# Kernel optimization log

Hardware: AMD Instinct MI355X
Metric: run time of the kernel (lower is better)

Reference implementation:

```python
import jax, jax.numpy as jnp
import numpy as np

N_NODES = 50000
N_EDGES = 1600000
D_IN = 192   # n_features + n_graphfea
D_HID = 128


def _gcn_conv(x, W, b, src, dst, dhis, n):
    """GCNConv returning two views.
    view1: symmetric-normalized propagation with self-loops (standard GCN).
    view2: raw neighbor sum of transformed features (to be scaled by D_inv outside).
    dhis: deg_hat^{-1/2} per node, deg_hat = in-degree + 1 (self loop).
    """
    h = x @ W + b                                      # [N, hid]
    w = dhis[src] * dhis[dst]                          # [E] edge norm
    view1 = jax.ops.segment_sum(h[src] * w[:, None], dst, num_segments=n)
    view1 = view1 + h * (dhis * dhis)[:, None]         # self-loop term
    view2 = jax.ops.segment_sum(h[src], dst, num_segments=n)
    return view1, view2


def setup_inputs() -> dict:
    key = jax.random.key(0)
    ks = jax.random.split(key, 12)
    x = jax.random.normal(ks[0], (N_NODES, D_IN), dtype=jnp.float32)
    view2 = jax.random.normal(ks[1], (N_NODES, D_IN), dtype=jnp.float32)
    edge_index = jax.random.randint(ks[2], (2, N_EDGES), 0, N_NODES, dtype=jnp.int64)
    D_inv = jax.random.uniform(ks[3], (N_NODES, 1), dtype=jnp.float32)
    def glorot(k, fan_in, fan_out):
        s = jnp.sqrt(jnp.float32(2.0 / (fan_in + fan_out)))
        return jax.random.normal(k, (fan_in, fan_out), dtype=jnp.float32) * s
    W1 = glorot(ks[4], D_IN, D_HID)
    W2 = glorot(ks[5], D_HID, D_HID)
    W3 = glorot(ks[6], D_HID, D_HID)
    W4 = glorot(ks[7], D_IN, D_HID)
    W5 = glorot(ks[8], D_HID, D_HID)
    W6 = glorot(ks[9], D_HID, D_HID)
    z = jnp.zeros((D_HID,), dtype=jnp.float32)
    return {"x": x, "view2": view2, "edge_index": edge_index, "D_inv": D_inv,
            "W1": W1, "b1": z, "W2": W2, "b2": z, "W3": W3, "b3": z,
            "W4": W4, "b4": z, "W5": W5, "b5": z, "W6": W6, "b6": z}


def reference(x, view2, edge_index, D_inv,
              W1, b1, W2, b2, W3, b3, W4, b4, W5, b5, W6, b6):
    n = x.shape[0]
    src, dst = edge_index[0], edge_index[1]
    deg = jax.ops.segment_sum(jnp.ones_like(dst, dtype=x.dtype), dst, num_segments=n)
    dhis = jax.lax.rsqrt(deg + 1.0)                    # deg_hat^{-1/2}
    relu = jax.nn.relu

    x1v1, x1v2 = _gcn_conv(x, W1, b1, src, dst, dhis, n)
    x2v1, x2v2 = _gcn_conv(view2, W4, b4, src, dst, dhis, n)
    x1 = relu(x1v1 + x2v2 * D_inv)
    x2 = relu(x2v1 + x1v2 * D_inv)

    z1v1, z1v2 = _gcn_conv(x1, W2, b2, src, dst, dhis, n)
    z2v1, z2v2 = _gcn_conv(x2, W5, b5, src, dst, dhis, n)
    z1 = relu(z1v1 + z2v2 * D_inv)
    z2 = relu(z2v1 + z1v2 * D_inv)

    v1v1, v1v2 = _gcn_conv(z1, W3, b3, src, dst, dhis, n)
    v2v1, v2v2 = _gcn_conv(z2, W6, b6, src, dst, dhis, n)
    v1 = relu(v1v1 + v2v2 * D_inv)
    v2 = relu(v2v1 + v1v2 * D_inv)

    q = jnp.concatenate([x1, z1, v1], axis=1)          # [N, 3*hid]
    p = jnp.concatenate([x2, z2, v2], axis=1)
    return q, p
```

## Files before the change

### kernel.cpp

```cpp
#include <hip/hip_runtime.h>

#define N_NODES 50000
#define N_EDGES 1600000
#define D_IN 192
#define D_HID 128

#define NSLICE 8
#define SLICE_SZ ((N_NODES + NSLICE - 1) / NSLICE)

typedef __bf16 bf16x8 __attribute__((ext_vector_type(8)));
typedef float f32x4 __attribute__((ext_vector_type(4)));
typedef float f32x2 __attribute__((ext_vector_type(2)));
typedef unsigned short u16x8 __attribute__((ext_vector_type(8)));

__device__ __forceinline__ unsigned short f2b(float x) {
    unsigned u = __builtin_bit_cast(unsigned, x);
    u += 0x7FFFu + ((u >> 16) & 1u);
    return (unsigned short)(u >> 16);
}
__device__ __forceinline__ float blo(unsigned u) {
    return __builtin_bit_cast(float, u << 16);
}
__device__ __forceinline__ float bhi(unsigned u) {
    return __builtin_bit_cast(float, u & 0xFFFF0000u);
}
__device__ __forceinline__ bf16x8 pack8(float4 a, float4 b) {
    u16x8 t;
    t[0] = f2b(a.x); t[1] = f2b(a.y); t[2] = f2b(a.z); t[3] = f2b(a.w);
    t[4] = f2b(b.x); t[5] = f2b(b.y); t[6] = f2b(b.z); t[7] = f2b(b.w);
    return __builtin_bit_cast(bf16x8, t);
}


__global__ void hist_kernel(const int* __restrict__ dst, int E,
                            int* __restrict__ cnt, int* __restrict__ rank) {
    int e = blockIdx.x * blockDim.x + threadIdx.x;
    if (e < E) rank[e] = atomicAdd(&cnt[dst[e]], 1);
}

__global__ __launch_bounds__(256) void scanA(const int* __restrict__ cnt,
                                             int* __restrict__ bsum, int n) {
    int i = blockIdx.x * 256 + threadIdx.x;
    int v = (i < n) ? cnt[i] : 0;
#pragma unroll
    for (int off = 32; off > 0; off >>= 1) v += __shfl_down(v, off);
    __shared__ int ws[4];
    if ((threadIdx.x & 63) == 0) ws[threadIdx.x >> 6] = v;
    __syncthreads();
    if (threadIdx.x == 0) bsum[blockIdx.x] = ws[0] + ws[1] + ws[2] + ws[3];
}

__global__ __launch_bounds__(256) void scanB(const int* __restrict__ bsum,
                                             int* __restrict__ boff,
                                             int* __restrict__ row_ptr, int nb, int n) {
    __shared__ int s[256];
    int tid = threadIdx.x;
    int v = (tid < nb) ? bsum[tid] : 0;
    s[tid] = v;
    __syncthreads();
    for (int off = 1; off < 256; off <<= 1) {
        int add = (tid >= off) ? s[tid - off] : 0;
        __syncthreads();
        s[tid] += add;
        __syncthreads();
    }
    if (tid < nb) boff[tid] = (tid > 0) ? s[tid - 1] : 0;
    if (tid == 0) row_ptr[n] = s[255];
}

__global__ __launch_bounds__(256) void scanC(const int* __restrict__ cnt,
                                             const int* __restrict__ boff,
                                             int* __restrict__ row_ptr,
                                             float* __restrict__ dhis, int n) {
    __shared__ int s[256];
    int tid = threadIdx.x;
    int i = blockIdx.x * 256 + tid;
    int c = (i < n) ? cnt[i] : 0;
    s[tid] = c;
    __syncthreads();
    for (int off = 1; off < 256; off <<= 1) {
        int add = (tid >= off) ? s[tid - off] : 0;
        __syncthreads();
        s[tid] += add;
        __syncthreads();
    }
    if (i < n) {
        int pre = boff[blockIdx.x] + s[tid] - c;
        row_ptr[i] = pre;
        dhis[i] = rsqrtf((float)c + 1.0f);
    }
}

__global__ __launch_bounds__(256) void fill_sliced(
        const int* __restrict__ src, const int* __restrict__ dst,
        const int* __restrict__ rank, const int* __restrict__ row_ptr,
        int* __restrict__ esrc, int E, int nchunks) {
    int slice = blockIdx.x & (NSLICE - 1);
    int chunk = blockIdx.x >> 3;
    int lo = slice * SLICE_SZ;
    int hi = lo + SLICE_SZ;
    int per = (E + nchunks - 1) / nchunks;
    int e0 = chunk * per;
    int e1 = min(e0 + per, E);
    for (int e = e0 + threadIdx.x; e < e1; e += 256) {
        int d = dst[e];
        if (d >= lo && d < hi) {
            esrc[row_ptr[d] + rank[e]] = src[e];
        }
    }
}


__global__ void prep_all(const float* __restrict__ W1, const float* __restrict__ W4,
                         const float* __restrict__ W2, const float* __restrict__ W3,
                         const float* __restrict__ W5, const float* __restrict__ W6,
                         unsigned short* __restrict__ Wt) {
    int idx = blockIdx.x * 256 + threadIdx.x;
    const float* W; int K, base;
    if      (idx <  24576) { W = W1; K = 192; base = 0; }
    else if (idx <  49152) { W = W4; K = 192; base = 24576; }
    else if (idx <  65536) { W = W2; K = 128; base = 49152; }
    else if (idx <  81920) { W = W3; K = 128; base = 65536; }
    else if (idx <  98304) { W = W5; K = 128; base = 81920; }
    else if (idx < 114688) { W = W6; K = 128; base = 98304; }
    else return;
    int r = idx - base;
    int j = r / K, k = r - j * K;
    Wt[idx] = f2b(W[(size_t)k * 128 + j]);
}


__global__ __launch_bounds__(256) void gemm_dual(
        const float* __restrict__ A0, const float* __restrict__ A1, int lda,
        int K, int ns,
        const unsigned short* __restrict__ Wt0, const unsigned short* __restrict__ Wt1,
        const float* __restrict__ bias0, const float* __restrict__ bias1,
        unsigned short* __restrict__ out, int M) {
    __shared__ __align__(16) unsigned short Wlds[192 * 128];

    int view = blockIdx.y;
    const float* A = view ? A1 : A0;
    const unsigned short* Wt = view ? Wt1 : Wt0;
    const float* bias = view ? bias1 : bias0;

    int tid = threadIdx.x;

    int nfrag = ns * 512;
    for (int f = tid; f < nfrag; f += 256) {
        int lane = f & 63;
        int gk = f >> 6;
        int g = gk / ns, ks = gk - g * ns;
        int col = g * 16 + (lane & 15);
        int kpos = ks * 32 + (lane >> 4) * 8;
        *(bf16x8*)(Wlds + (size_t)f * 8) =
            *(const bf16x8*)(Wt + (size_t)col * K + kpos);
    }
    __syncthreads();

    int wave = tid >> 6, lane = tid & 63;
    int m = lane & 15, quad = lane >> 4;
    int row0 = blockIdx.x * 128;

    int rA0 = row0 + wave * 32 + m;
    int rA1 = rA0 + 16;
    int cA0 = rA0 < M ? rA0 : M - 1;
    int cA1 = rA1 < M ? rA1 : M - 1;
    const float* a0 = A + (size_t)cA0 * lda + quad * 8;
    const float* a1 = A + (size_t)cA1 * lda + quad * 8;

    f32x4 acc[2][8];
#pragma unroll
    for (int h = 0; h < 2; ++h)
#pragma unroll
        for (int g = 0; g < 8; ++g) acc[h][g] = (f32x4){0.f, 0.f, 0.f, 0.f};

    const bf16x8* wl = (const bf16x8*)Wlds;
    for (int ks = 0; ks < ns; ++ks) {
        float4 va = *(const float4*)(a0 + ks * 32);
        float4 vb = *(const float4*)(a0 + ks * 32 + 4);
        float4 vc = *(const float4*)(a1 + ks * 32);
        float4 vd = *(const float4*)(a1 + ks * 32 + 4);
        bf16x8 af0 = pack8(va, vb);
        bf16x8 af1 = pack8(vc, vd);
#pragma unroll
        for (int g = 0; g < 8; ++g) {
            bf16x8 bfr = wl[(g * ns + ks) * 64 + lane];
            acc[0][g] = __builtin_amdgcn_mfma_f32_16x16x32_bf16(af0, bfr, acc[0][g], 0, 0, 0);
            acc[1][g] = __builtin_amdgcn_mfma_f32_16x16x32_bf16(af1, bfr, acc[1][g], 0, 0, 0);
        }
    }

#pragma unroll
    for (int h = 0; h < 2; ++h) {
#pragma unroll
        for (int g = 0; g < 8; ++g) {
            int col = g * 16 + m;
            float bv = bias[col];
            int ci = ((col >> 1) << 2) + (view << 1) + (col & 1);
#pragma unroll
            for (int r = 0; r < 4; ++r) {
                int grow = row0 + wave * 32 + h * 16 + quad * 4 + r;
                if (grow < M) out[(size_t)grow * 256 + ci] = f2b(acc[h][g][r] + bv);
            }
        }
    }
}


__global__ __launch_bounds__(256) void agg_kernel(
        const unsigned* __restrict__ hcomb,
        const int* __restrict__ row_ptr, const int* __restrict__ esrc,
        const float* __restrict__ dhis, const float* __restrict__ D_inv,
        float* __restrict__ out_q, float* __restrict__ out_p, int n) {
    int wave = threadIdx.x >> 6, lane = threadIdx.x & 63;
    int d = blockIdx.x * 4 + wave;
    if (d >= n) return;

    const uint2* hc2 = (const uint2*)hcomb;

    int e0 = row_ptr[d], e1 = row_ptr[d + 1];
    f32x2 a1 = {0.f, 0.f}, g1 = {0.f, 0.f};
    f32x2 a2 = {0.f, 0.f}, g2 = {0.f, 0.f};

#define EDGE_BODY(u, w) {                                         \
        f32x2 v1 = {blo((u).x), bhi((u).x)};                      \
        f32x2 v2 = {blo((u).y), bhi((u).y)};                      \
        f32x2 wv = {(w), (w)};                                    \
        a1 += v1; g1 = __builtin_elementwise_fma(v1, wv, g1);     \
        a2 += v2; g2 = __builtin_elementwise_fma(v2, wv, g2); }

    int e = e0;
    for (; e + 8 <= e1; e += 8) {
        int4 sa = *(const int4*)(esrc + e);
        int4 sb = *(const int4*)(esrc + e + 4);
        uint2 u0 = hc2[((size_t)sa.x << 6) + lane];
        uint2 u1 = hc2[((size_t)sa.y << 6) + lane];
        uint2 u2 = hc2[((size_t)sa.z << 6) + lane];
        uint2 u3 = hc2[((size_t)sa.w << 6) + lane];
        uint2 u4 = hc2[((size_t)sb.x << 6) + lane];
        uint2 u5 = hc2[((size_t)sb.y << 6) + lane];
        uint2 u6 = hc2[((size_t)sb.z << 6) + lane];
        uint2 u7 = hc2[((size_t)sb.w << 6) + lane];
        float w0 = dhis[sa.x], w1 = dhis[sa.y], w2 = dhis[sa.z], w3 = dhis[sa.w];
        float w4 = dhis[sb.x], w5 = dhis[sb.y], w6 = dhis[sb.z], w7 = dhis[sb.w];
        EDGE_BODY(u0, w0); EDGE_BODY(u1, w1);
        EDGE_BODY(u2, w2); EDGE_BODY(u3, w3);
        EDGE_BODY(u4, w4); EDGE_BODY(u5, w5);
        EDGE_BODY(u6, w6); EDGE_BODY(u7, w7);
    }
    for (; e + 4 <= e1; e += 4) {
        int4 sa = *(const int4*)(esrc + e);
        uint2 u0 = hc2[((size_t)sa.x << 6) + lane];
        uint2 u1 = hc2[((size_t)sa.y << 6) + lane];
        uint2 u2 = hc2[((size_t)sa.z << 6) + lane];
        uint2 u3 = hc2[((size_t)sa.w << 6) + lane];
        float w0 = dhis[sa.x], w1 = dhis[sa.y], w2 = dhis[sa.z], w3 = dhis[sa.w];
        EDGE_BODY(u0, w0); EDGE_BODY(u1, w1);
        EDGE_BODY(u2, w2); EDGE_BODY(u3, w3);
    }
    for (; e < e1; ++e) {
        int s = esrc[e];
        uint2 u = hc2[((size_t)s << 6) + lane];
        EDGE_BODY(u, dhis[s]);
    }
#undef EDGE_BODY

    float dh = dhis[d];
    float di = D_inv[d];
    float dh2 = dh * dh;
    f32x2 dhv = {dh, dh}, dh2v = {dh2, dh2}, div = {di, di};

    uint2 us = hc2[((size_t)d << 6) + lane];
    f32x2 s1 = {blo(us.x), bhi(us.x)};
    f32x2 s2 = {blo(us.y), bhi(us.y)};

    f32x2 o1 = __builtin_elementwise_fma(g1, dhv,
               __builtin_elementwise_fma(s1, dh2v, a2 * div));
    f32x2 o2 = __builtin_elementwise_fma(g2, dhv,
               __builtin_elementwise_fma(s2, dh2v, a1 * div));

    f32x2 zero = {0.f, 0.f};
    o1 = __builtin_elementwise_max(o1, zero);
    o2 = __builtin_elementwise_max(o2, zero);
    *(f32x2*)(out_q + (size_t)d * 384 + lane * 2) = o1;
    *(f32x2*)(out_p + (size_t)d * 384 + lane * 2) = o2;
}


extern "C" void kernel_launch(void* const* d_in, const int* in_sizes, int n_in,
                              void* d_out, int out_size, void* d_ws, size_t ws_size,
                              hipStream_t stream) {
    const float* x     = (const float*)d_in[0];
    const float* view2 = (const float*)d_in[1];
    const int*   eidx  = (const int*)d_in[2];
    const float* D_inv = (const float*)d_in[3];
    const float* W1 = (const float*)d_in[4];  const float* b1 = (const float*)d_in[5];
    const float* W2 = (const float*)d_in[6];  const float* b2 = (const float*)d_in[7];
    const float* W3 = (const float*)d_in[8];  const float* b3 = (const float*)d_in[9];
    const float* W4 = (const float*)d_in[10]; const float* b4 = (const float*)d_in[11];
    const float* W5 = (const float*)d_in[12]; const float* b5 = (const float*)d_in[13];
    const float* W6 = (const float*)d_in[14]; const float* b6 = (const float*)d_in[15];

    const int n = N_NODES;
    const int E = N_EDGES;
    const int* src  = eidx;
    const int* dstv = eidx + E;

    char* ws = (char*)d_ws;
    size_t off = 0;
    auto alloc = [&](size_t bytes) -> void* {
        void* p = ws + off;
        off += (bytes + 255) & ~(size_t)255;
        return p;
    };
    int*   cnt     = (int*)alloc((size_t)n * 4);
    int*   row_ptr = (int*)alloc((size_t)(n + 1) * 4);
    float* dhis    = (float*)alloc((size_t)n * 4);
    int*   rank    = (int*)alloc((size_t)E * 4);
    int*   esrc    = (int*)alloc((size_t)E * 4);
    int*   bsum    = (int*)alloc((size_t)256 * 4);
    int*   boff    = (int*)alloc((size_t)256 * 4);
    unsigned short* hcomb = (unsigned short*)alloc((size_t)n * 256 * 2);
    unsigned short* Wta   = (unsigned short*)alloc((size_t)114688 * 2);

    unsigned short* Wt1 = Wta + 0;
    unsigned short* Wt4 = Wta + 24576;
    unsigned short* Wt2 = Wta + 49152;
    unsigned short* Wt3 = Wta + 65536;
    unsigned short* Wt5 = Wta + 81920;
    unsigned short* Wt6 = Wta + 98304;

    float* qb = (float*)d_out;
    float* pb = qb + (size_t)n * 384;

    hipMemsetAsync(cnt, 0, (size_t)n * 4, stream);
    int eblocks = (E + 255) / 256;
    int nb = (n + 255) / 256;
    hist_kernel<<<eblocks, 256, 0, stream>>>(dstv, E, cnt, rank);
    scanA<<<nb, 256, 0, stream>>>(cnt, bsum, n);
    scanB<<<1, 256, 0, stream>>>(bsum, boff, row_ptr, nb, n);
    scanC<<<nb, 256, 0, stream>>>(cnt, boff, row_ptr, dhis, n);
    int nchunks = 1024;
    fill_sliced<<<nchunks * NSLICE, 256, 0, stream>>>(src, dstv, rank, row_ptr,
                                                      esrc, E, nchunks);

    prep_all<<<(114688 + 255) / 256, 256, 0, stream>>>(W1, W4, W2, W3, W5, W6, Wta);

    dim3 ggrid((n + 127) / 128, 2);
    int ablocks = (n + 3) / 4;
    const unsigned* hc = (const unsigned*)hcomb;

    gemm_dual<<<ggrid, 256, 0, stream>>>(x, view2, D_IN, 192, 6, Wt1, Wt4, b1, b4, hcomb, n);
    agg_kernel<<<ablocks, 256, 0, stream>>>(hc, row_ptr, esrc, dhis, D_inv, qb + 0, pb + 0, n);

    gemm_dual<<<ggrid, 256, 0, stream>>>(qb, pb, 384, 128, 4, Wt2, Wt5, b2, b5, hcomb, n);
    agg_kernel<<<ablocks, 256, 0, stream>>>(hc, row_ptr, esrc, dhis, D_inv, qb + 128, pb + 128, n);

    gemm_dual<<<ggrid, 256, 0, stream>>>(qb + 128, pb + 128, 384, 128, 4, Wt3, Wt6, b3, b6, hcomb, n);
    agg_kernel<<<ablocks, 256, 0, stream>>>(hc, row_ptr, esrc, dhis, D_inv, qb + 256, pb + 256, n);
}
```

Baseline: 778.5 us.

## Fuse CSR construction and weight prep into one cooperative kernel

Replaces the memset, histogram, three scan kernels, the sliced fill and the weight transpose with one cooperative kernel of 1024 blocks that uses grid-wide syncs between phases. The goal is to cut kernel launch overhead and the dependency gaps between the small preprocessing kernels. It also precomputes each edge's absolute CSR slot before the fill, so the sliced fill filters on slot range instead of reading row_ptr again. The risks are the cost of several grid syncs and the lower parallelism of the fill phase, which now has 1024 blocks instead of 8192.

```diff
diff --git a/kernel.cpp b/kernel.cpp
--- a/kernel.cpp
+++ b/kernel.cpp
@@ -1,4 +1,7 @@
 #include <hip/hip_runtime.h>
+#include <hip/hip_cooperative_groups.h>
+
+namespace cg = cooperative_groups;
 
 #define N_NODES 50000
 #define N_EDGES 1600000
@@ -7,6 +10,10 @@
 
 #define NSLICE 8
 #define SLICE_SZ ((N_NODES + NSLICE - 1) / NSLICE)
+
+#define CSR_BLOCKS 1024
+#define CHUNK ((N_NODES + CSR_BLOCKS - 1) / CSR_BLOCKS)
+#define NW_TOTAL 114688
 
 typedef __bf16 bf16x8 __attribute__((ext_vector_type(8)));
 typedef float f32x4 __attribute__((ext_vector_type(4)));
@@ -32,101 +39,118 @@
 }
 
 
-__global__ void hist_kernel(const int* __restrict__ dst, int E,
-                            int* __restrict__ cnt, int* __restrict__ rank) {
-    int e = blockIdx.x * blockDim.x + threadIdx.x;
-    if (e < E) rank[e] = atomicAdd(&cnt[dst[e]], 1);
-}
-
-__global__ __launch_bounds__(256) void scanA(const int* __restrict__ cnt,
-                                             int* __restrict__ bsum, int n) {
-    int i = blockIdx.x * 256 + threadIdx.x;
-    int v = (i < n) ? cnt[i] : 0;
-#pragma unroll
-    for (int off = 32; off > 0; off >>= 1) v += __shfl_down(v, off);
+__global__ __launch_bounds__(256) void csr_build(
+        const int* __restrict__ src, const int* __restrict__ dst,
+        const float* __restrict__ W1, const float* __restrict__ W4,
+        const float* __restrict__ W2, const float* __restrict__ W3,
+        const float* __restrict__ W5, const float* __restrict__ W6,
+        unsigned short* __restrict__ Wt,
+        int* __restrict__ cnt, int* __restrict__ rank,
+        int* __restrict__ row_ptr, float* __restrict__ dhis,
+        int* __restrict__ bsum, int* __restrict__ esrc) {
+    cg::grid_group grid = cg::this_grid();
+    int tid = threadIdx.x, bid = blockIdx.x;
+    int gtid = bid * 256 + tid;
+    const int gstride = CSR_BLOCKS * 256;
+
+    __shared__ int ls[256];
     __shared__ int ws[4];
-    if ((threadIdx.x & 63) == 0) ws[threadIdx.x >> 6] = v;
-    __syncthreads();
-    if (threadIdx.x == 0) bsum[blockIdx.x] = ws[0] + ws[1] + ws[2] + ws[3];
-}
-
-__global__ __launch_bounds__(256) void scanB(const int* __restrict__ bsum,
-                                             int* __restrict__ boff,
-                                             int* __restrict__ row_ptr, int nb, int n) {
-    __shared__ int s[256];
-    int tid = threadIdx.x;
-    int v = (tid < nb) ? bsum[tid] : 0;
-    s[tid] = v;
-    __syncthreads();
-    for (int off = 1; off < 256; off <<= 1) {
-        int add = (tid >= off) ? s[tid - off] : 0;
+
+    for (int i = gtid; i < N_NODES; i += gstride) cnt[i] = 0;
+    for (int idx = gtid; idx < NW_TOTAL; idx += gstride) {
+        const float* W; int K, base;
+        if      (idx <  24576) { W = W1; K = 192; base = 0; }
+        else if (idx <  49152) { W = W4; K = 192; base = 24576; }
+        else if (idx <  65536) { W = W2; K = 128; base = 49152; }
+        else if (idx <  81920) { W = W3; K = 128; base = 65536; }
+        else if (idx <  98304) { W = W5; K = 128; base = 81920; }
+        else                   { W = W6; K = 128; base = 98304; }
+        int r = idx - base;
+        int j = r / K, k = r - j * K;
+        Wt[idx] = f2b(W[(size_t)k * 128 + j]);
+    }
+    grid.sync();
+
+    for (int e = gtid; e < N_EDGES; e += gstride)
+        rank[e] = atomicAdd(&cnt[dst[e]], 1);
+    grid.sync();
+
+    {
+        int s = 0;
+        int base = bid * CHUNK;
+        for (int i = tid; i < CHUNK; i += 256) {
+            int j = base + i;
+            if (j < N_NODES) s += cnt[j];
+        }
+#pragma unroll
+        for (int off = 32; off > 0; off >>= 1) s += __shfl_down(s, off);
+        if ((tid & 63) == 0) ws[tid >> 6] = s;
         __syncthreads();
-        s[tid] += add;
+        if (tid == 0) bsum[bid] = ws[0] + ws[1] + ws[2] + ws[3];
+    }
+    grid.sync();
+
+    if (bid == 0) {
+        int v[4];
+        int base = tid * 4;
+        int s = 0;
+#pragma unroll
+        for (int k = 0; k < 4; ++k) { v[k] = bsum[base + k]; s += v[k]; }
+        ls[tid] = s;
         __syncthreads();
-    }
-    if (tid < nb) boff[tid] = (tid > 0) ? s[tid - 1] : 0;
-    if (tid == 0) row_ptr[n] = s[255];
-}
-
-__global__ __launch_bounds__(256) void scanC(const int* __restrict__ cnt,
-                                             const int* __restrict__ boff,
-                                             int* __restrict__ row_ptr,
-                                             float* __restrict__ dhis, int n) {
-    __shared__ int s[256];
-    int tid = threadIdx.x;
-    int i = blockIdx.x * 256 + tid;
-    int c = (i < n) ? cnt[i] : 0;
-    s[tid] = c;
-    __syncthreads();
-    for (int off = 1; off < 256; off <<= 1) {
-        int add = (tid >= off) ? s[tid - off] : 0;
+        for (int off = 1; off < 256; off <<= 1) {
+            int add = (tid >= off) ? ls[tid - off] : 0;
+            __syncthreads();
+            ls[tid] += add;
+            __syncthreads();
+        }
+        int pre = (tid > 0) ? ls[tid - 1] : 0;
+#pragma unroll
+        for (int k = 0; k < 4; ++k) { int t = v[k]; bsum[base + k] = pre; pre += t; }
+        if (tid == 0) row_ptr[N_NODES] = N_EDGES;
+    }
+    grid.sync();
+
+    {
+        int base = bid * CHUNK;
+        int j = base + tid;
+        int c = (tid < CHUNK && j < N_NODES) ? cnt[j] : 0;
+        ls[tid] = c;
         __syncthreads();
-        s[tid] += add;
-        __syncthreads();
-    }
-    if (i < n) {
-        int pre = boff[blockIdx.x] + s[tid] - c;
-        row_ptr[i] = pre;
-        dhis[i] = rsqrtf((float)c + 1.0f);
-    }
-}
-
-__global__ __launch_bounds__(256) void fill_sliced(
-        const int* __restrict__ src, const int* __restrict__ dst,
-        const int* __restrict__ rank, const int* __restrict__ row_ptr,
-        int* __restrict__ esrc, int E, int nchunks) {
-    int slice = blockIdx.x & (NSLICE - 1);
-    int chunk = blockIdx.x >> 3;
-    int lo = slice * SLICE_SZ;
-    int hi = lo + SLICE_SZ;
-    int per = (E + nchunks - 1) / nchunks;
-    int e0 = chunk * per;
-    int e1 = min(e0 + per, E);
-    for (int e = e0 + threadIdx.x; e < e1; e += 256) {
-        int d = dst[e];
-        if (d >= lo && d < hi) {
-            esrc[row_ptr[d] + rank[e]] = src[e];
-        }
-    }
-}
-
-
-__global__ void prep_all(const float* __restrict__ W1, const float* __restrict__ W4,
-                         const float* __restrict__ W2, const float* __restrict__ W3,
-                         const float* __restrict__ W5, const float* __restrict__ W6,
-                         unsigned short* __restrict__ Wt) {
-    int idx = blockIdx.x * 256 + threadIdx.x;
-    const float* W; int K, base;
-    if      (idx <  24576) { W = W1; K = 192; base = 0; }
-    else if (idx <  49152) { W = W4; K = 192; base = 24576; }
-    else if (idx <  65536) { W = W2; K = 128; base = 49152; }
-    else if (idx <  81920) { W = W3; K = 128; base = 65536; }
-    else if (idx <  98304) { W = W5; K = 128; base = 81920; }
-    else if (idx < 114688) { W = W6; K = 128; base = 98304; }
-    else return;
-    int r = idx - base;
-    int j = r / K, k = r - j * K;
-    Wt[idx] = f2b(W[(size_t)k * 128 + j]);
+        for (int off = 1; off < 64; off <<= 1) {
+            int add = (tid >= off) ? ls[tid - off] : 0;
+            __syncthreads();
+            ls[tid] += add;
+            __syncthreads();
+        }
+        if (tid < CHUNK && j < N_NODES) {
+            int pre = bsum[bid] + ls[tid] - c;
+            row_ptr[j] = pre;
+            dhis[j] = rsqrtf((float)c + 1.0f);
+        }
+    }
+    grid.sync();
+
+    for (int e = gtid; e < N_EDGES; e += gstride)
+        rank[e] = row_ptr[dst[e]] + rank[e];
+    grid.sync();
+
+    {
+        int slice = bid & (NSLICE - 1);
+        int chunk = bid >> 3;
+        int hi_node = (slice + 1) * SLICE_SZ;
+        if (hi_node > N_NODES) hi_node = N_NODES;
+        int slo = row_ptr[slice * SLICE_SZ];
+        int shi = row_ptr[hi_node];
+        const int nch = CSR_BLOCKS / NSLICE;
+        int per = (N_EDGES + nch - 1) / nch;
+        int e0 = chunk * per;
+        int e1 = min(e0 + per, N_EDGES);
+        for (int e = e0 + tid; e < e1; e += 256) {
+            int sl = rank[e];
+            if (sl >= slo && sl < shi) esrc[sl] = src[e];
+        }
+    }
 }
 
 
@@ -302,9 +326,8 @@
     const float* W6 = (const float*)d_in[14]; const float* b6 = (const float*)d_in[15];
 
     const int n = N_NODES;
-    const int E = N_EDGES;
     const int* src  = eidx;
-    const int* dstv = eidx + E;
+    const int* dstv = eidx + N_EDGES;
 
     char* ws = (char*)d_ws;
     size_t off = 0;
@@ -316,12 +339,11 @@
     int*   cnt     = (int*)alloc((size_t)n * 4);
     int*   row_ptr = (int*)alloc((size_t)(n + 1) * 4);
     float* dhis    = (float*)alloc((size_t)n * 4);
-    int*   rank    = (int*)alloc((size_t)E * 4);
-    int*   esrc    = (int*)alloc((size_t)E * 4);
-    int*   bsum    = (int*)alloc((size_t)256 * 4);
-    int*   boff    = (int*)alloc((size_t)256 * 4);
+    int*   rank    = (int*)alloc((size_t)N_EDGES * 4);
+    int*   esrc    = (int*)alloc((size_t)N_EDGES * 4);
+    int*   bsum    = (int*)alloc((size_t)CSR_BLOCKS * 4);
     unsigned short* hcomb = (unsigned short*)alloc((size_t)n * 256 * 2);
-    unsigned short* Wta   = (unsigned short*)alloc((size_t)114688 * 2);
+    unsigned short* Wta   = (unsigned short*)alloc((size_t)NW_TOTAL * 2);
 
     unsigned short* Wt1 = Wta + 0;
     unsigned short* Wt4 = Wta + 24576;
@@ -333,18 +355,17 @@
     float* qb = (float*)d_out;
     float* pb = qb + (size_t)n * 384;
 
-    hipMemsetAsync(cnt, 0, (size_t)n * 4, stream);
-    int eblocks = (E + 255) / 256;
-    int nb = (n + 255) / 256;
-    hist_kernel<<<eblocks, 256, 0, stream>>>(dstv, E, cnt, rank);
-    scanA<<<nb, 256, 0, stream>>>(cnt, bsum, n);
-    scanB<<<1, 256, 0, stream>>>(bsum, boff, row_ptr, nb, n);
-    scanC<<<nb, 256, 0, stream>>>(cnt, boff, row_ptr, dhis, n);
-    int nchunks = 1024;
-    fill_sliced<<<nchunks * NSLICE, 256, 0, stream>>>(src, dstv, rank, row_ptr,
-                                                      esrc, E, nchunks);
-
-    prep_all<<<(114688 + 255) / 256, 256, 0, stream>>>(W1, W4, W2, W3, W5, W6, Wta);
+    {
+        void* args[] = {
+            (void*)&src, (void*)&dstv,
+            (void*)&W1, (void*)&W4, (void*)&W2, (void*)&W3, (void*)&W5, (void*)&W6,
+            (void*)&Wta,
+            (void*)&cnt, (void*)&rank, (void*)&row_ptr, (void*)&dhis,
+            (void*)&bsum, (void*)&esrc
+        };
+        hipLaunchCooperativeKernel((const void*)csr_build, dim3(CSR_BLOCKS),
+                                   dim3(256), args, 0, stream);
+    }
 
     dim3 ggrid((n + 127) / 128, 2);
     int ablocks = (n + 3) / 4;
```

After: 1.423 ms. 82.8% more time.
